# Kernel tuning notes

Hardware: AMD Instinct MI355X
Metric: run time of the kernel (lower is better)

The kernel has to match this reference:

```python
import jax, jax.numpy as jnp
import numpy as np

LS = 16000      # FFT length = ceil(L/stride)*stride with L=16000, stride=128
STRIDE = 128    # decimation hop
B, C, L, K = 32, 40, 16000, 128


def setup_inputs() -> dict:
    key = jax.random.key(0)
    k1, k2, k3 = jax.random.split(key, 3)
    x = jax.random.normal(k1, (B, 1, L), dtype=jnp.float32)
    kernels_real = jax.random.normal(k2, (C, K), dtype=jnp.float32)
    kernels_imag = jax.random.normal(k3, (C, K), dtype=jnp.float32)
    return {"x": x, "kernels_real": kernels_real, "kernels_imag": kernels_imag}


def reference(x, kernels_real, kernels_imag):
    # Complex analysis filters (C, K); zero-padded to LS inside fft via n=LS
    kernels = kernels_real + 1j * kernels_imag
    Xf = jnp.fft.fft(x, n=LS, axis=-1)                     # (B, 1, LS) complex
    Kf = jnp.fft.fft(kernels, n=LS, axis=-1)[None, :, :]   # (1, C, LS) complex
    y = jnp.fft.ifft(Xf * Kf, n=LS, axis=-1)               # (B, C, LS) circular conv
    return y[:, :, ::STRIDE]                               # (B, C, LS//STRIDE) complex
```

## Files before the change

kernel.cpp:

```cpp
#include <hip/hip_runtime.h>

#define BB     32
#define CC     40
#define LL     16000
#define KK     128
#define MM     125
#define KPAD2  129
#define NOUT   (BB * CC * MM)

__global__ __launch_bounds__(256) void ISAC_conv_kernel(
    const float* __restrict__ x,
    const float* __restrict__ kr,
    const float* __restrict__ ki,
    float*       __restrict__ out,
    int mode)
{
    __shared__ float2 skc[CC * KPAD2];

    for (int i = threadIdx.x; i < CC * KK; i += 256) {
        int c = i >> 7;
        int k = i & 127;
        skc[c * KPAD2 + k] = make_float2(kr[i], ki[i]);
    }
    __syncthreads();

    int id = blockIdx.x * 256 + threadIdx.x;
    int c  = id % CC;
    int t  = id / CC;
    int m  = t % MM;
    int b  = t / MM;

    const float2* kc = skc + c * KPAD2;
    const float*  xb = x + b * LL;
    const int base = m * KK;

    const float* p = xb + (m == 0 ? LL : base);

    float2 k0  = kc[0];
    float  xv0 = xb[base];
    float accr = xv0 * k0.x;
    float acci = xv0 * k0.y;

#pragma unroll
    for (int j = 1; j < KK; ++j) {
        float  xv = p[-j];
        float2 kv = kc[j];
        accr = fmaf(xv, kv.x, accr);
        acci = fmaf(xv, kv.y, acci);
    }

    int oidx = (b * CC + c) * MM + m;
    if (mode == 0) {
        out[oidx]        = accr;
        out[NOUT + oidx] = acci;
    } else if (mode == 1) {
        out[oidx] = accr;
    } else {
        reinterpret_cast<float2*>(out)[oidx] = make_float2(accr, acci);
    }
}

extern "C" void kernel_launch(void* const* d_in, const int* in_sizes, int n_in,
                              void* d_out, int out_size, void* d_ws, size_t ws_size,
                              hipStream_t stream) {
    const float* x  = (const float*)d_in[0];
    const float* kr = (const float*)d_in[1];
    const float* ki = (const float*)d_in[2];
    float* out = (float*)d_out;

    int mode;
    if (out_size == 2 * NOUT)      mode = 0;
    else if (out_size == NOUT)     mode = 1;
    else                           mode = 2;

    const int total = NOUT;
    const int block = 256;
    const int grid  = (total + block - 1) / block;

    ISAC_conv_kernel<<<grid, block, 0, stream>>>(x, kr, ki, out, mode);
}
```

Measured before the change: 63.02 us.

## Compute two decimated outputs per thread and vectorize input loads

Each thread now computes two output positions (m and m+62), sharing the LDS kernel-coefficient reads between them, and loads input samples as float2 pairs. The coefficient staging loop also uses vectorized loads, and the block size drops to 128. This cuts LDS traffic per output and adds independent accumulation chains. The cost is fewer total threads, fewer waves to hide latency, and one duplicated output at m=62.

Result: no change. 62.91 us (-0.2%).

```diff
diff --git a/kernel.cpp b/kernel.cpp
--- a/kernel.cpp
+++ b/kernel.cpp
@@ -1,14 +1,17 @@
 #include <hip/hip_runtime.h>
 
-#define BB     32
-#define CC     40
-#define LL     16000
-#define KK     128
-#define MM     125
-#define KPAD2  129
-#define NOUT   (BB * CC * MM)
+#define BB      32
+#define CC      40
+#define LL      16000
+#define KK      128
+#define MM      125
+#define KPAD2   129
+#define NOUT    (BB * CC * MM)
+#define MSLOTS  63
+#define BLK     128
+#define NTHR    (BB * MSLOTS * CC)
 
-__global__ __launch_bounds__(256) void ISAC_conv_kernel(
+__global__ __launch_bounds__(BLK) void ISAC_conv_kernel(
     const float* __restrict__ x,
     const float* __restrict__ kr,
     const float* __restrict__ ki,
@@ -17,46 +20,62 @@
 {
     __shared__ float2 skc[CC * KPAD2];
 
-    for (int i = threadIdx.x; i < CC * KK; i += 256) {
-        int c = i >> 7;
-        int k = i & 127;
-        skc[c * KPAD2 + k] = make_float2(kr[i], ki[i]);
+    for (int i = threadIdx.x; i < CC * KK / 2; i += BLK) {
+        int c  = i >> 6;
+        int jp = (i & 63) << 1;
+        float2 r2 = *reinterpret_cast<const float2*>(kr + c * KK + jp);
+        float2 i2 = *reinterpret_cast<const float2*>(ki + c * KK + jp);
+        skc[c * KPAD2 + jp]     = make_float2(r2.x, i2.x);
+        skc[c * KPAD2 + jp + 1] = make_float2(r2.y, i2.y);
     }
     __syncthreads();
 
-    int id = blockIdx.x * 256 + threadIdx.x;
+    int id = blockIdx.x * BLK + threadIdx.x;
     int c  = id % CC;
-    int t  = id / CC;
-    int m  = t % MM;
-    int b  = t / MM;
+    int s  = id / CC;
+    int m1 = s % MSLOTS;
+    int b  = s / MSLOTS;
+    int m2 = m1 + 62;
 
     const float2* kc = skc + c * KPAD2;
     const float*  xb = x + b * LL;
-    const int base = m * KK;
+    const int base1 = m1 * KK, base2 = m2 * KK;
+    const float* p1 = xb + (m1 == 0 ? LL : base1);
+    const float* p2 = xb + base2;
 
-    const float* p = xb + (m == 0 ? LL : base);
-
-    float2 k0  = kc[0];
-    float  xv0 = xb[base];
-    float accr = xv0 * k0.x;
-    float acci = xv0 * k0.y;
+    float2 k0 = kc[0];
+    float xv1 = xb[base1], xv2 = xb[base2];
+    float ar1 = xv1 * k0.x, ai1 = xv1 * k0.y;
+    float ar2 = xv2 * k0.x, ai2 = xv2 * k0.y;
 
 #pragma unroll
-    for (int j = 1; j < KK; ++j) {
-        float  xv = p[-j];
-        float2 kv = kc[j];
-        accr = fmaf(xv, kv.x, accr);
-        acci = fmaf(xv, kv.y, acci);
+    for (int jo = 1; jo < KK - 1; jo += 2) {
+        float2 xp1 = *reinterpret_cast<const float2*>(p1 - jo - 1);
+        float2 xp2 = *reinterpret_cast<const float2*>(p2 - jo - 1);
+        float2 ka  = kc[jo];
+        float2 kb2 = kc[jo + 1];
+        ar1 = fmaf(xp1.y, ka.x,  ar1);  ai1 = fmaf(xp1.y, ka.y,  ai1);
+        ar2 = fmaf(xp2.y, ka.x,  ar2);  ai2 = fmaf(xp2.y, ka.y,  ai2);
+        ar1 = fmaf(xp1.x, kb2.x, ar1);  ai1 = fmaf(xp1.x, kb2.y, ai1);
+        ar2 = fmaf(xp2.x, kb2.x, ar2);  ai2 = fmaf(xp2.x, kb2.y, ai2);
+    }
+    {
+        float xt1 = p1[-(KK - 1)], xt2 = p2[-(KK - 1)];
+        float2 kl = kc[KK - 1];
+        ar1 = fmaf(xt1, kl.x, ar1);  ai1 = fmaf(xt1, kl.y, ai1);
+        ar2 = fmaf(xt2, kl.x, ar2);  ai2 = fmaf(xt2, kl.y, ai2);
     }
 
-    int oidx = (b * CC + c) * MM + m;
+    int o1 = (b * CC + c) * MM + m1;
+    int o2 = (b * CC + c) * MM + m2;
     if (mode == 0) {
-        out[oidx]        = accr;
-        out[NOUT + oidx] = acci;
+        out[o1]        = ar1;  out[NOUT + o1] = ai1;
+        out[o2]        = ar2;  out[NOUT + o2] = ai2;
     } else if (mode == 1) {
-        out[oidx] = accr;
+        out[o1] = ar1;  out[o2] = ar2;
     } else {
-        reinterpret_cast<float2*>(out)[oidx] = make_float2(accr, acci);
+        reinterpret_cast<float2*>(out)[o1] = make_float2(ar1, ai1);
+        reinterpret_cast<float2*>(out)[o2] = make_float2(ar2, ai2);
     }
 }
 
@@ -73,9 +92,6 @@
     else if (out_size == NOUT)     mode = 1;
     else                           mode = 2;
 
-    const int total = NOUT;
-    const int block = 256;
-    const int grid  = (total + block - 1) / block;
-
-    ISAC_conv_kernel<<<grid, block, 0, stream>>>(x, kr, ki, out, mode);
+    const int grid = NTHR / BLK;
+    ISAC_conv_kernel<<<grid, BLK, 0, stream>>>(x, kr, ki, out, mode);
 }
```
